# Kernel tuning notes

Hardware: AMD Instinct MI355X
Metric: run time of the kernel (lower is better)

The kernel has to match this reference:

```python
import jax, jax.numpy as jnp
import numpy as np

EMBED = 1024

def setup_inputs() -> dict:
    key = jax.random.key(0)
    ks = jax.random.split(key, 10)
    B, S, E = 4, 2048, EMBED
    inv = 1.0 / np.sqrt(E)
    return {
        "query": jax.random.normal(ks[0], (B, S, E), jnp.float32),
        "key": jax.random.normal(ks[1], (B, S, E), jnp.float32),
        "value": jax.random.normal(ks[2], (B, S, E), jnp.float32),
        "attn_mask": jnp.zeros((B, S, S), jnp.float32),
        "Wq": jax.random.normal(ks[3], (E, E), jnp.float32) * inv,
        "bq": jnp.zeros((E,), jnp.float32),
        "Wk": jax.random.normal(ks[4], (E, E), jnp.float32) * inv,
        "bk": jnp.zeros((E,), jnp.float32),
        "Wv": jax.random.normal(ks[5], (E, E), jnp.float32) * inv,
        "bv": jnp.zeros((E,), jnp.float32),
    }

def reference(query, key, value, attn_mask, Wq, bq, Wk, bk, Wv, bv):
    E = query.shape[-1]
    q = query @ Wq.T + bq            # [B,S,E]
    k = key @ Wk.T + bk              # [B,S,E]
    v = value @ Wv.T + bv            # [B,S,E]
    scores = jnp.einsum('bse,bte->bst', q, k) / jnp.sqrt(jnp.float32(E))
    scores = scores + attn_mask      # [B,S,S]
    attn = jax.nn.softmax(scores, axis=-1)
    return jnp.einsum('bst,bte->bse', attn, v)
```

## Files before the change

kernel.cpp:

```cpp
#include <hip/hip_runtime.h>
#include <cstdint>
#include <cstddef>

typedef __bf16 bf16;
typedef __bf16 bf16x8 __attribute__((ext_vector_type(8)));
typedef float  f32x4  __attribute__((ext_vector_type(4)));

#define NB 4
#define SS 2048
#define EE 1024

#define BUFB   24576
#define LDS3   (3 * BUFB)
#define BUFB64 49152
#define LDS64  (3 * BUFB64)

static __device__ __forceinline__ void glds16(const bf16* g, void* l)
{
    __builtin_amdgcn_global_load_lds(
        (const __attribute__((address_space(1))) unsigned int*)g,
        (__attribute__((address_space(3))) unsigned int*)l,
        16, 0, 0);
}

static __device__ __forceinline__ void swz_block(int& bx, int& by, int& bz)
{
    const int nx = gridDim.x, ny = gridDim.y;
    const int nwg = nx * ny * gridDim.z;
    int lin = blockIdx.x + nx * (blockIdx.y + ny * blockIdx.z);
    const int per = nwg >> 3;
    lin = (lin & 7) * per + (lin >> 3);
    bz = lin / (nx * ny);
    const int r = lin - bz * nx * ny;
    by = r / nx;
    bx = r - by * nx;
}

static __device__ __forceinline__ void kloop32(
    const bf16* __restrict__ A, const bf16* __restrict__ Bm,
    int lda, int ldb, int nt, char* lds, int m0, int n0, int tid,
    f32x4 acc[4][4])
{
    constexpr int NBUF = 3;
    const int lane = tid & 63, w = tid >> 6;
    const int wm = w >> 2, wn = w & 3;
    const int lr = lane & 15, kq = lane >> 4;
    const int cb = ((kq ^ ((lr >> 1) & 3)) << 4);

    const int srow   = tid >> 2;
    const int chunkL = (tid & 3) ^ ((srow >> 1) & 3);
    const bf16* Asrc = A  + (size_t)(m0 + srow) * lda + chunkL * 8;
    const bf16* Bsrc = Bm + (size_t)(n0 + srow) * ldb + chunkL * 8;
    const int wofs = w << 10;

#pragma unroll
    for (int p = 0; p < NBUF - 1; ++p) {
        char* d = lds + p * BUFB + wofs;
        const int kt = p * 32;
        glds16(Asrc + kt,                     d);
        glds16(Bsrc + kt,                     d + 8192);
        glds16(Bsrc + (size_t)128 * ldb + kt, d + 16384);
    }
    asm volatile("s_waitcnt vmcnt(3)" ::: "memory");
    __builtin_amdgcn_sched_barrier(0);
    __builtin_amdgcn_s_barrier();
    __builtin_amdgcn_sched_barrier(0);

    int rb = 0, sb = NBUF - 1;
    for (int t = 0; t < nt; ++t) {
        char* la = lds + rb * BUFB;
        char* lb = la + 8192;
        const int ts = (t + NBUF - 1 < nt) ? t + NBUF - 1 : nt - 1;
        const int kt = ts * 32;
        char* d = lds + sb * BUFB + wofs;

        bf16x8 af[4], bg[4];
#pragma unroll
        for (int m = 0; m < 4; ++m)
            af[m] = *(const bf16x8*)(la + (wm * 64 + m * 16 + lr) * 64 + cb);
#pragma unroll
        for (int n = 0; n < 4; ++n)
            bg[n] = *(const bf16x8*)(lb + (wn * 64 + n * 16 + lr) * 64 + cb);

        glds16(Asrc + kt,                     d);
        glds16(Bsrc + kt,                     d + 8192);
        glds16(Bsrc + (size_t)128 * ldb + kt, d + 16384);

        __builtin_amdgcn_s_setprio(1);
#pragma unroll
        for (int m = 0; m < 4; ++m)
#pragma unroll
            for (int n = 0; n < 4; ++n)
                acc[m][n] = __builtin_amdgcn_mfma_f32_16x16x32_bf16(af[m], bg[n], acc[m][n], 0, 0, 0);
        __builtin_amdgcn_s_setprio(0);

        if (t < nt - 1) {
            asm volatile("s_waitcnt vmcnt(3)" ::: "memory");
            __builtin_amdgcn_sched_barrier(0);
            __builtin_amdgcn_s_barrier();
            __builtin_amdgcn_sched_barrier(0);
        }
        rb = (rb + 1 == NBUF) ? 0 : rb + 1;
        sb = (sb + 1 == NBUF) ? 0 : sb + 1;
    }
    asm volatile("s_waitcnt vmcnt(0)" ::: "memory");
}

static __device__ __forceinline__ void kloop64(
    const bf16* __restrict__ A, const bf16* __restrict__ Bm,
    int lda, int ldb, int nt, char* lds, int m0, int n0, int tid,
    f32x4 acc[4][4])
{
    const int lane = tid & 63, w = tid >> 6;
    const int wm = w >> 2, wn = w & 3;
    const int lr = lane & 15, kq = lane >> 4;
    const int axor = (lr & 7) << 4;

    const int srow   = tid >> 3;
    const int chunkL = (tid & 7) ^ (srow & 7);
    const bf16* Asrc = A  + (size_t)(m0 + srow) * lda + chunkL * 8;
    const bf16* Bsrc = Bm + (size_t)(n0 + srow) * ldb + chunkL * 8;
    const int wofs = w << 10;

#pragma unroll
    for (int p = 0; p < 2; ++p) {
        char* d = lds + p * BUFB64 + wofs;
        const int kt = p * 64;
        glds16(Asrc + kt,                        d);
        glds16(Asrc + (size_t)64 * lda + kt,     d + 8192);
        glds16(Bsrc + kt,                        d + 16384);
        glds16(Bsrc + (size_t)64 * ldb + kt,     d + 16384 + 8192);
        glds16(Bsrc + (size_t)128 * ldb + kt,    d + 16384 + 16384);
        glds16(Bsrc + (size_t)192 * ldb + kt,    d + 16384 + 24576);
    }
    asm volatile("s_waitcnt vmcnt(6)" ::: "memory");
    __builtin_amdgcn_sched_barrier(0);
    __builtin_amdgcn_s_barrier();
    __builtin_amdgcn_sched_barrier(0);

    for (int t = 0; t < nt; ++t) {
        char* la = lds + (t % 3) * BUFB64;
        char* lb = la + 16384;
        char* sa = lds + ((t + 2) % 3) * BUFB64;
        const bool st = (t + 2) < nt;
        const int kt = (t + 2) * 64;

        bf16x8 af[4], bg[4];
        {
            const int cbk = (kq * 16) ^ axor;
#pragma unroll
            for (int m = 0; m < 4; ++m)
                af[m] = *(const bf16x8*)(la + (wm * 64 + m * 16 + lr) * 128 + cbk);
#pragma unroll
            for (int n = 0; n < 4; ++n)
                bg[n] = *(const bf16x8*)(lb + (wn * 64 + n * 16 + lr) * 128 + cbk);
            if (st) {
                glds16(Asrc + kt,                    sa + wofs);
                glds16(Asrc + (size_t)64 * lda + kt, sa + 8192 + wofs);
                glds16(Bsrc + kt,                    sa + 16384 + wofs);
            }
            __builtin_amdgcn_s_setprio(1);
#pragma unroll
            for (int m = 0; m < 4; ++m)
#pragma unroll
                for (int n = 0; n < 4; ++n)
                    acc[m][n] = __builtin_amdgcn_mfma_f32_16x16x32_bf16(af[m], bg[n], acc[m][n], 0, 0, 0);
            __builtin_amdgcn_s_setprio(0);
        }
        {
            const int cbk = (64 + kq * 16) ^ axor;
#pragma unroll
            for (int m = 0; m < 4; ++m)
                af[m] = *(const bf16x8*)(la + (wm * 64 + m * 16 + lr) * 128 + cbk);
#pragma unroll
            for (int n = 0; n < 4; ++n)
                bg[n] = *(const bf16x8*)(lb + (wn * 64 + n * 16 + lr) * 128 + cbk);
            if (st) {
                glds16(Bsrc + (size_t)64 * ldb + kt,  sa + 16384 + 8192 + wofs);
                glds16(Bsrc + (size_t)128 * ldb + kt, sa + 16384 + 16384 + wofs);
                glds16(Bsrc + (size_t)192 * ldb + kt, sa + 16384 + 24576 + wofs);
            }
            __builtin_amdgcn_s_setprio(1);
#pragma unroll
            for (int m = 0; m < 4; ++m)
#pragma unroll
                for (int n = 0; n < 4; ++n)
                    acc[m][n] = __builtin_amdgcn_mfma_f32_16x16x32_bf16(af[m], bg[n], acc[m][n], 0, 0, 0);
            __builtin_amdgcn_s_setprio(0);
        }
        if (t < nt - 1) {
            if (st) { asm volatile("s_waitcnt vmcnt(6)" ::: "memory"); }
            else    { asm volatile("s_waitcnt vmcnt(0)" ::: "memory"); }
            __builtin_amdgcn_sched_barrier(0);
            __builtin_amdgcn_s_barrier();
            __builtin_amdgcn_sched_barrier(0);
        }
    }
}

__global__ __launch_bounds__(256) void cvt_all(
    const float* __restrict__ q, const float* __restrict__ k, const float* __restrict__ v,
    const float* __restrict__ Wq, const float* __restrict__ Wk, const float* __restrict__ Wv,
    bf16* __restrict__ qc, bf16* __restrict__ kc, bf16* __restrict__ vc,
    bf16* __restrict__ Wc)
{
    const int y = blockIdx.y;
    const float* s; bf16* d; size_t i;
    if (blockIdx.x < 4096) {
        s = (y == 0) ? q : (y == 1) ? k : v;
        d = (y == 0) ? qc : (y == 1) ? kc : vc;
        i = ((size_t)blockIdx.x * 256 + threadIdx.x) * 8;
    } else {
        s = (y == 0) ? Wq : (y == 1) ? Wk : Wv;
        d = Wc + (size_t)y * EE * EE;
        i = ((size_t)(blockIdx.x - 4096) * 256 + threadIdx.x) * 8;
    }
    const float4 f0 = *(const float4*)(s + i);
    const float4 f1 = *(const float4*)(s + i + 4);
    bf16x8 h;
    h[0] = (bf16)f0.x; h[1] = (bf16)f0.y; h[2] = (bf16)f0.z; h[3] = (bf16)f0.w;
    h[4] = (bf16)f1.x; h[5] = (bf16)f1.y; h[6] = (bf16)f1.z; h[7] = (bf16)f1.w;
    *(bf16x8*)(d + i) = h;
}

__global__ __launch_bounds__(512, 4) void proj8(
    const bf16* __restrict__ qc, const bf16* __restrict__ kc, const bf16* __restrict__ vc,
    const bf16* __restrict__ Wc,
    const float* __restrict__ bq, const float* __restrict__ bk, const float* __restrict__ bv,
    bf16* __restrict__ qb, bf16* __restrict__ kb, bf16* __restrict__ vt)
{
    extern __shared__ char lds[];
    int bx, by, bz; swz_block(bx, by, bz);
    const bf16* A; const float* bias;
    if (bz == 0)      { A = qc; bias = bq; }
    else if (bz == 1) { A = kc; bias = bk; }
    else              { A = vc; bias = bv; }
    const bf16* Bm = Wc + (size_t)bz * EE * EE;

    const int m0 = by * 128, n0 = bx * 256;
    const int tid = threadIdx.x;

    f32x4 acc[4][4];
#pragma unroll
    for (int m = 0; m < 4; ++m)
#pragma unroll
        for (int n = 0; n < 4; ++n) { acc[m][n][0] = 0.f; acc[m][n][1] = 0.f; acc[m][n][2] = 0.f; acc[m][n][3] = 0.f; }

    kloop32(A, Bm, EE, EE, EE / 32, lds, m0, n0, tid, acc);

    const int lane = tid & 63, w = tid >> 6, wm = w >> 2, wn = w & 3;
    const int lr = lane & 15, kq = lane >> 4;

    if (bz < 2) {
        bf16* out = (bz == 0) ? qb : kb;
#pragma unroll
        for (int n = 0; n < 4; ++n) {
            const int gcol = n0 + wn * 64 + n * 16 + lr;
            const float bb = bias[gcol];
#pragma unroll
            for (int m = 0; m < 4; ++m)
#pragma unroll
                for (int j = 0; j < 4; ++j) {
                    const int grow = m0 + wm * 64 + m * 16 + kq * 4 + j;
                    out[(size_t)grow * EE + gcol] = (bf16)(acc[m][n][j] + bb);
                }
        }
    } else {
        __syncthreads();
#pragma unroll
        for (int n = 0; n < 4; ++n) {
            const int gc = wn * 64 + n * 16 + lr;
            const float bb = bias[n0 + gc];
#pragma unroll
            for (int m = 0; m < 4; ++m) {
                const int gr = wm * 64 + m * 16 + kq * 4;
                union { unsigned short u[4]; uint2 v; } h;
#pragma unroll
                for (int j = 0; j < 4; ++j) {
                    union { bf16 b; unsigned short u; } cv;
                    cv.b = (bf16)(acc[m][n][j] + bb);
                    h.u[j] = cv.u;
                }
                char* p = lds + gc * 256 + (((gr >> 3) ^ (gc & 7)) << 4) + (gr & 7) * 2;
                *(uint2*)p = h.v;
            }
        }
        __syncthreads();
        const int r = tid >> 1, par = tid & 1;
        const int bb_ = m0 >> 11;
        const int s0 = m0 & (SS - 1);
        bf16* dst = vt + ((size_t)bb_ * EE + n0 + r) * SS + s0 + par * 64;
#pragma unroll
        for (int i = 0; i < 8; ++i) {
            const int c = par * 8 + i;
            const char* p = lds + r * 256 + ((c ^ (r & 7)) << 4);
            *(uint4*)&dst[i * 8] = *(const uint4*)p;
        }
    }
}

__global__ __launch_bounds__(512, 4) void scores8(const bf16* __restrict__ qb,
                                                  const bf16* __restrict__ kb,
                                                  const float* __restrict__ mask,
                                                  bf16* __restrict__ sc)
{
    extern __shared__ char lds[];
    int bx, by, bz; swz_block(bx, by, bz);
    const bf16* A  = qb + (size_t)bz * SS * EE;
    const bf16* Bm = kb + (size_t)bz * SS * EE;

    const int m0 = by * 128, n0 = bx * 256;
    const int tid = threadIdx.x;

    f32x4 acc[4][4];
#pragma unroll
    for (int m = 0; m < 4; ++m)
#pragma unroll
        for (int n = 0; n < 4; ++n) { acc[m][n][0] = 0.f; acc[m][n][1] = 0.f; acc[m][n][2] = 0.f; acc[m][n][3] = 0.f; }

    kloop32(A, Bm, EE, EE, EE / 32, lds, m0, n0, tid, acc);

    const int lane = tid & 63, w = tid >> 6, wm = w >> 2, wn = w & 3;
    const int lr = lane & 15, kq = lane >> 4;
    const float* mrow = mask + (size_t)bz * SS * SS;
    bf16* out = sc + (size_t)bz * SS * SS;
    const float scale = 0.03125f;
#pragma unroll
    for (int m = 0; m < 4; ++m)
#pragma unroll
        for (int n = 0; n < 4; ++n)
#pragma unroll
            for (int j = 0; j < 4; ++j) {
                const int grow = m0 + wm * 64 + m * 16 + kq * 4 + j;
                const int gcol = n0 + wn * 64 + n * 16 + lr;
                const float v = acc[m][n][j] * scale + mrow[(size_t)grow * SS + gcol];
                out[(size_t)grow * SS + gcol] = (bf16)v;
            }
}

__global__ __launch_bounds__(256) void softmax_kernel(bf16* __restrict__ sc)
{
    __shared__ float red[4];
    const size_t row = blockIdx.x;
    uint4* rp = (uint4*)(sc + row * (size_t)SS);
    const int tid = threadIdx.x, lane = tid & 63, wid = tid >> 6;

    const uint4 d = rp[tid];
    const unsigned int u[4] = { d.x, d.y, d.z, d.w };
    float f[8];
#pragma unroll
    for (int i = 0; i < 4; ++i) {
        union { unsigned int i_; float f_; } lo, hi;
        lo.i_ = u[i] << 16;
        hi.i_ = u[i] & 0xffff0000u;
        f[2 * i]     = lo.f_;
        f[2 * i + 1] = hi.f_;
    }

    float m = f[0];
#pragma unroll
    for (int i = 1; i < 8; ++i) m = fmaxf(m, f[i]);
#pragma unroll
    for (int o = 32; o > 0; o >>= 1) m = fmaxf(m, __shfl_xor(m, o));
    if (lane == 0) red[wid] = m;
    __syncthreads();
    m = fmaxf(fmaxf(red[0], red[1]), fmaxf(red[2], red[3]));
    __syncthreads();

    float e[8], s = 0.f;
#pragma unroll
    for (int i = 0; i < 8; ++i) { e[i] = __expf(f[i] - m); s += e[i]; }
#pragma unroll
    for (int o = 32; o > 0; o >>= 1) s += __shfl_xor(s, o);
    if (lane == 0) red[wid] = s;
    __syncthreads();
    s = red[0] + red[1] + red[2] + red[3];
    const float inv = 1.0f / s;

    unsigned int ou[4];
#pragma unroll
    for (int i = 0; i < 4; ++i) {
        union { bf16 h; unsigned short b; } a0, a1;
        a0.h = (bf16)(e[2 * i] * inv);
        a1.h = (bf16)(e[2 * i + 1] * inv);
        ou[i] = ((unsigned int)a1.b << 16) | (unsigned int)a0.b;
    }
    rp[tid] = make_uint4(ou[0], ou[1], ou[2], ou[3]);
}

__global__ __launch_bounds__(512) void pv8(const bf16* __restrict__ sc,
                                           const bf16* __restrict__ vt,
                                           float* __restrict__ outp)
{
    extern __shared__ char lds[];
    int bx, by, bz; swz_block(bx, by, bz);
    const bf16* A  = sc + (size_t)bz * SS * SS;
    const bf16* Bm = vt + (size_t)bz * EE * SS;

    const int m0 = by * 128, n0 = bx * 256;
    const int tid = threadIdx.x;

    f32x4 acc[4][4];
#pragma unroll
    for (int m = 0; m < 4; ++m)
#pragma unroll
        for (int n = 0; n < 4; ++n) { acc[m][n][0] = 0.f; acc[m][n][1] = 0.f; acc[m][n][2] = 0.f; acc[m][n][3] = 0.f; }

    kloop64(A, Bm, SS, SS, SS / 64, lds, m0, n0, tid, acc);

    const int lane = tid & 63, w = tid >> 6, wm = w >> 2, wn = w & 3;
    const int lr = lane & 15, kq = lane >> 4;
#pragma unroll
    for (int m = 0; m < 4; ++m)
#pragma unroll
        for (int n = 0; n < 4; ++n)
#pragma unroll
            for (int j = 0; j < 4; ++j) {
                const int grow = m0 + wm * 64 + m * 16 + kq * 4 + j;
                const int gcol = n0 + wn * 64 + n * 16 + lr;
                outp[((size_t)bz * SS + grow) * EE + gcol] = acc[m][n][j];
            }
}

extern "C" void kernel_launch(void* const* d_in, const int* in_sizes, int n_in,
                              void* d_out, int out_size, void* d_ws, size_t ws_size,
                              hipStream_t stream)
{
    const float* query = (const float*)d_in[0];
    const float* key_  = (const float*)d_in[1];
    const float* value = (const float*)d_in[2];
    const float* mask  = (const float*)d_in[3];
    const float* Wq = (const float*)d_in[4];
    const float* bq = (const float*)d_in[5];
    const float* Wk = (const float*)d_in[6];
    const float* bk = (const float*)d_in[7];
    const float* Wv = (const float*)d_in[8];
    const float* bv = (const float*)d_in[9];
    float* outp = (float*)d_out;

    char* ws = (char*)d_ws;
    const size_t QKV = (size_t)NB * SS * EE * 2;
    const size_t SCB = (size_t)NB * SS * SS * 2;
    const size_t WCB = (size_t)3 * EE * EE * 2;
    if (ws_size < 4 * QKV + SCB + WCB) return;

    bf16* qb = (bf16*)(ws);
    bf16* kb = (bf16*)(ws + QKV);
    bf16* vt = (bf16*)(ws + 3 * QKV);
    bf16* sc = (bf16*)(ws + 4 * QKV);
    bf16* Wc = (bf16*)(ws + 4 * QKV + SCB);
    bf16* qc = (bf16*)(ws + 2 * QKV);
    bf16* kc = sc;
    bf16* vc = (bf16*)(ws + 5 * QKV);

    (void)hipFuncSetAttribute((const void*)proj8,   hipFuncAttributeMaxDynamicSharedMemorySize, LDS3);
    (void)hipFuncSetAttribute((const void*)scores8, hipFuncAttributeMaxDynamicSharedMemorySize, LDS3);
    (void)hipFuncSetAttribute((const void*)pv8,     hipFuncAttributeMaxDynamicSharedMemorySize, LDS64);

    dim3 blk(256), blk5(512);
    cvt_all<<<dim3(4096 + 512, 3), blk, 0, stream>>>(
        query, key_, value, Wq, Wk, Wv, qc, kc, vc, Wc);

    proj8<<<dim3(EE / 256, (NB * SS) / 128, 3), blk5, LDS3, stream>>>(
        qc, kc, vc, Wc, bq, bk, bv, qb, kb, vt);
    scores8<<<dim3(SS / 256, SS / 128, NB), blk5, LDS3, stream>>>(qb, kb, mask, sc);
    softmax_kernel<<<dim3(NB * SS), blk, 0, stream>>>(sc);
    pv8<<<dim3(EE / 256, SS / 128, NB), blk5, LDS64, stream>>>(sc, vt, outp);
}
```

Measured before the change: 194.2 us.

## Fuse fp32-to-bf16 activation conversion into projection GEMM A-tile loading

The separate conversion pass over query/key/value is removed. The projection GEMM instead reads fp32 activations straight from global memory into registers, converts them to bf16 and writes them into the swizzled LDS tile, prefetching three stages ahead. Only the weights are still pre-converted by a small kernel. This drops a full read and write of the bf16 activation copies, but each projection block now reads fp32 A data, twice the bytes, through register loads rather than direct-to-LDS loads, and this is repeated across the four N-tiles.

```diff
diff --git a/kernel.cpp b/kernel.cpp
--- a/kernel.cpp
+++ b/kernel.cpp
@@ -36,6 +36,14 @@
     bx = r - by * nx;
 }
 
+static __device__ __forceinline__ bf16x8 cvt8(float4 f0, float4 f1)
+{
+    bf16x8 h;
+    h[0] = (bf16)f0.x; h[1] = (bf16)f0.y; h[2] = (bf16)f0.z; h[3] = (bf16)f0.w;
+    h[4] = (bf16)f1.x; h[5] = (bf16)f1.y; h[6] = (bf16)f1.z; h[7] = (bf16)f1.w;
+    return h;
+}
+
 static __device__ __forceinline__ void kloop32(
     const bf16* __restrict__ A, const bf16* __restrict__ Bm,
     int lda, int ldb, int nt, char* lds, int m0, int n0, int tid,
@@ -96,6 +104,89 @@
 
         if (t < nt - 1) {
             asm volatile("s_waitcnt vmcnt(3)" ::: "memory");
+            __builtin_amdgcn_sched_barrier(0);
+            __builtin_amdgcn_s_barrier();
+            __builtin_amdgcn_sched_barrier(0);
+        }
+        rb = (rb + 1 == NBUF) ? 0 : rb + 1;
+        sb = (sb + 1 == NBUF) ? 0 : sb + 1;
+    }
+    asm volatile("s_waitcnt vmcnt(0)" ::: "memory");
+}
+
+static __device__ __forceinline__ void kloop32f(
+    const float* __restrict__ A, const bf16* __restrict__ Bm,
+    int lda, int ldb, int nt, char* lds, int m0, int n0, int tid,
+    f32x4 acc[4][4])
+{
+    constexpr int NBUF = 3;
+    const int lane = tid & 63, w = tid >> 6;
+    const int wm = w >> 2, wn = w & 3;
+    const int lr = lane & 15, kq = lane >> 4;
+    const int cb = ((kq ^ ((lr >> 1) & 3)) << 4);
+
+    const int srow   = tid >> 2;
+    const int cL     = tid & 3;
+    const int pchunk = cL ^ ((srow >> 1) & 3);
+    const int chunkL = cL ^ ((srow >> 1) & 3);
+    const float* Af  = A + (size_t)(m0 + srow) * lda + cL * 8;
+    const bf16* Bsrc = Bm + (size_t)(n0 + srow) * ldb + chunkL * 8;
+    const int wofs = w << 10;
+    const int aw   = srow * 64 + pchunk * 16;
+
+    {
+        const float4* s0 = (const float4*)(Af + 0);
+        *(bf16x8*)(lds + 0 * BUFB + aw) = cvt8(s0[0], s0[1]);
+        glds16(Bsrc + 0,                     lds + 0 * BUFB + wofs + 8192);
+        glds16(Bsrc + (size_t)128 * ldb + 0, lds + 0 * BUFB + wofs + 16384);
+    }
+    const float4* s2 = (const float4*)(Af + 2 * 32);
+    float4 ra0 = s2[0], ra1 = s2[1];
+    {
+        const float4* s1 = (const float4*)(Af + 32);
+        *(bf16x8*)(lds + 1 * BUFB + aw) = cvt8(s1[0], s1[1]);
+        glds16(Bsrc + 32,                     lds + 1 * BUFB + wofs + 8192);
+        glds16(Bsrc + (size_t)128 * ldb + 32, lds + 1 * BUFB + wofs + 16384);
+    }
+    asm volatile("s_waitcnt vmcnt(4) lgkmcnt(0)" ::: "memory");
+    __builtin_amdgcn_sched_barrier(0);
+    __builtin_amdgcn_s_barrier();
+    __builtin_amdgcn_sched_barrier(0);
+
+    int rb = 0, sb = NBUF - 1;
+    for (int t = 0; t < nt; ++t) {
+        char* la = lds + rb * BUFB;
+        char* lb = la + 8192;
+        const int ts  = (t + 2 < nt) ? t + 2 : nt - 1;
+        const int ts3 = (t + 3 < nt) ? t + 3 : nt - 1;
+        char* d = lds + sb * BUFB;
+
+        bf16x8 af[4], bg[4];
+#pragma unroll
+        for (int m = 0; m < 4; ++m)
+            af[m] = *(const bf16x8*)(la + (wm * 64 + m * 16 + lr) * 64 + cb);
+#pragma unroll
+        for (int n = 0; n < 4; ++n)
+            bg[n] = *(const bf16x8*)(lb + (wn * 64 + n * 16 + lr) * 64 + cb);
+
+        *(bf16x8*)(d + aw) = cvt8(ra0, ra1);
+        {
+            const float4* sn = (const float4*)(Af + ts3 * 32);
+            ra0 = sn[0]; ra1 = sn[1];
+        }
+        glds16(Bsrc + ts * 32,                     d + wofs + 8192);
+        glds16(Bsrc + (size_t)128 * ldb + ts * 32, d + wofs + 16384);
+
+        __builtin_amdgcn_s_setprio(1);
+#pragma unroll
+        for (int m = 0; m < 4; ++m)
+#pragma unroll
+            for (int n = 0; n < 4; ++n)
+                acc[m][n] = __builtin_amdgcn_mfma_f32_16x16x32_bf16(af[m], bg[n], acc[m][n], 0, 0, 0);
+        __builtin_amdgcn_s_setprio(0);
+
+        if (t < nt - 1) {
+            asm volatile("s_waitcnt vmcnt(4) lgkmcnt(0)" ::: "memory");
             __builtin_amdgcn_sched_barrier(0);
             __builtin_amdgcn_s_barrier();
             __builtin_amdgcn_sched_barrier(0);
@@ -198,43 +289,32 @@
     }
 }
 
-__global__ __launch_bounds__(256) void cvt_all(
-    const float* __restrict__ q, const float* __restrict__ k, const float* __restrict__ v,
+__global__ __launch_bounds__(256) void cvt_w(
     const float* __restrict__ Wq, const float* __restrict__ Wk, const float* __restrict__ Wv,
-    bf16* __restrict__ qc, bf16* __restrict__ kc, bf16* __restrict__ vc,
     bf16* __restrict__ Wc)
 {
     const int y = blockIdx.y;
-    const float* s; bf16* d; size_t i;
-    if (blockIdx.x < 4096) {
-        s = (y == 0) ? q : (y == 1) ? k : v;
-        d = (y == 0) ? qc : (y == 1) ? kc : vc;
-        i = ((size_t)blockIdx.x * 256 + threadIdx.x) * 8;
-    } else {
-        s = (y == 0) ? Wq : (y == 1) ? Wk : Wv;
-        d = Wc + (size_t)y * EE * EE;
-        i = ((size_t)(blockIdx.x - 4096) * 256 + threadIdx.x) * 8;
-    }
+    const float* s = (y == 0) ? Wq : (y == 1) ? Wk : Wv;
+    bf16* d = Wc + (size_t)y * EE * EE;
+    const size_t i = ((size_t)blockIdx.x * 256 + threadIdx.x) * 8;
     const float4 f0 = *(const float4*)(s + i);
     const float4 f1 = *(const float4*)(s + i + 4);
-    bf16x8 h;
-    h[0] = (bf16)f0.x; h[1] = (bf16)f0.y; h[2] = (bf16)f0.z; h[3] = (bf16)f0.w;
-    h[4] = (bf16)f1.x; h[5] = (bf16)f1.y; h[6] = (bf16)f1.z; h[7] = (bf16)f1.w;
-    *(bf16x8*)(d + i) = h;
+    *(bf16x8*)(d + i) = cvt8(f0, f1);
 }
 
 __global__ __launch_bounds__(512, 4) void proj8(
-    const bf16* __restrict__ qc, const bf16* __restrict__ kc, const bf16* __restrict__ vc,
+    const float* __restrict__ query, const float* __restrict__ key_,
+    const float* __restrict__ value,
     const bf16* __restrict__ Wc,
     const float* __restrict__ bq, const float* __restrict__ bk, const float* __restrict__ bv,
     bf16* __restrict__ qb, bf16* __restrict__ kb, bf16* __restrict__ vt)
 {
     extern __shared__ char lds[];
     int bx, by, bz; swz_block(bx, by, bz);
-    const bf16* A; const float* bias;
-    if (bz == 0)      { A = qc; bias = bq; }
-    else if (bz == 1) { A = kc; bias = bk; }
-    else              { A = vc; bias = bv; }
+    const float* A; const float* bias;
+    if (bz == 0)      { A = query; bias = bq; }
+    else if (bz == 1) { A = key_;  bias = bk; }
+    else              { A = value; bias = bv; }
     const bf16* Bm = Wc + (size_t)bz * EE * EE;
 
     const int m0 = by * 128, n0 = bx * 256;
@@ -246,7 +326,7 @@
 #pragma unroll
         for (int n = 0; n < 4; ++n) { acc[m][n][0] = 0.f; acc[m][n][1] = 0.f; acc[m][n][2] = 0.f; acc[m][n][3] = 0.f; }
 
-    kloop32(A, Bm, EE, EE, EE / 32, lds, m0, n0, tid, acc);
+    kloop32f(A, Bm, EE, EE, EE / 32, lds, m0, n0, tid, acc);
 
     const int lane = tid & 63, w = tid >> 6, wm = w >> 2, wn = w & 3;
     const int lr = lane & 15, kq = lane >> 4;
@@ -449,20 +529,16 @@
     bf16* vt = (bf16*)(ws + 3 * QKV);
     bf16* sc = (bf16*)(ws + 4 * QKV);
     bf16* Wc = (bf16*)(ws + 4 * QKV + SCB);
-    bf16* qc = (bf16*)(ws + 2 * QKV);
-    bf16* kc = sc;
-    bf16* vc = (bf16*)(ws + 5 * QKV);
 
     (void)hipFuncSetAttribute((const void*)proj8,   hipFuncAttributeMaxDynamicSharedMemorySize, LDS3);
     (void)hipFuncSetAttribute((const void*)scores8, hipFuncAttributeMaxDynamicSharedMemorySize, LDS3);
     (void)hipFuncSetAttribute((const void*)pv8,     hipFuncAttributeMaxDynamicSharedMemorySize, LDS64);
 
     dim3 blk(256), blk5(512);
-    cvt_all<<<dim3(4096 + 512, 3), blk, 0, stream>>>(
-        query, key_, value, Wq, Wk, Wv, qc, kc, vc, Wc);
+    cvt_w<<<dim3(512, 3), blk, 0, stream>>>(Wq, Wk, Wv, Wc);
 
     proj8<<<dim3(EE / 256, (NB * SS) / 128, 3), blk5, LDS3, stream>>>(
-        qc, kc, vc, Wc, bq, bk, bv, qb, kb, vt);
+        query, key_, value, Wc, bq, bk, bv, qb, kb, vt);
     scores8<<<dim3(SS / 256, SS / 128, NB), blk5, LDS3, stream>>>(qb, kb, mask, sc);
     softmax_kernel<<<dim3(NB * SS), blk, 0, stream>>>(sc);
     pv8<<<dim3(EE / 256, SS / 128, NB), blk5, LDS64, stream>>>(sc, vt, outp);
```

Measured after the change: 200.2 us. +3.1%, slower.
